# Optimization experiments

Hardware: AMD Instinct MI355X
Metric: run time of the kernel (lower is better)

Reference implementation:

```python
import jax, jax.numpy as jnp
import numpy as np
from jax import lax

SLOPE = 0.01  # nn.LeakyReLU default negative slope

def leaky(x):
    return jnp.where(x >= 0, x, SLOPE * x)

def conv2d(x, w, b, pad):
    # x: [N,C,H,W], w: [O,I,kh,kw]
    y = lax.conv_general_dilated(x, w, (1, 1), [(pad, pad), (pad, pad)],
                                 dimension_numbers=('NCHW', 'OIHW', 'NCHW'))
    return y + b[None, :, None, None]

def centered_ifftn(x, axes):
    # np.fft.fftshift(np.fft.ifftn(np.fft.ifftshift(X), norm='ortho'))
    return jnp.fft.fftshift(jnp.fft.ifftn(jnp.fft.ifftshift(x, axes=axes), axes=axes, norm='ortho'), axes=axes)

def setup_inputs() -> dict:
    key = jax.random.key(0)
    ks = jax.random.split(key, 10)
    B, H, W, CK = 8, 640, 368, 32
    return {
        'img':    jax.random.normal(ks[0], (B, 1, H, W), jnp.float32),
        'kspace': jax.random.normal(ks[1], (B, 2, H, W), jnp.float32),
        # k_model1: Conv2d(2, CK, 3, padding=1) + LeakyReLU
        'wk': jax.random.normal(ks[2], (CK, 2, 3, 3), jnp.float32) * 0.1,
        'bk': jnp.zeros((CK,), jnp.float32),
        # conv1: Conv2d(CK, 2, kernel_size=1)
        'w1': jax.random.normal(ks[3], (2, CK, 1, 1), jnp.float32) * 0.1,
        'b1': jnp.zeros((2,), jnp.float32),
        # conv2: Conv2d(2, 1, kernel_size=1)
        'w2': jax.random.normal(ks[4], (1, 2, 1, 1), jnp.float32) * 0.1,
        'b2': jnp.zeros((1,), jnp.float32),
        # i_model1: Conv2d(1, 1, 3, padding=1) + LeakyReLU
        'wi': jax.random.normal(ks[5], (1, 1, 3, 3), jnp.float32) * 0.1,
        'bi': jnp.zeros((1,), jnp.float32),
    }

def reference(img, kspace, wk, bk, w1, b1, w2, b2, wi, bi):
    # k-space branch: k_model1 then conv1 + LeakyReLU
    out1 = leaky(conv2d(leaky(conv2d(kspace, wk, bk, 1)), w1, b1, 0))  # [B,2,H,W]
    # channel 0 = real, channel 1 = imag; ifftn over ALL axes (incl. batch),
    # exactly as the original numpy call with axes=range(out.ndim)
    cplx = out1[:, 0].astype(jnp.complex64) + 1j * out1[:, 1].astype(jnp.complex64)  # [B,H,W]
    im = jnp.abs(centered_ifftn(cplx, (0, 1, 2)))[:, None]  # [B,1,H,W]
    # concat with image, cast to half (torch.cuda.HalfTensor), conv2 + LeakyReLU
    out = jnp.concatenate([im, img], axis=1).astype(jnp.float16)  # [B,2,H,W]
    out = leaky(conv2d(out, w2.astype(jnp.float16), b2.astype(jnp.float16), 0))
    out = out.astype(jnp.float32)  # [B,1,H,W]
    # image-domain model
    return leaky(conv2d(out, wi, bi, 1))  # [B,1,H,W]
```

## Files before the change

kernel.cpp:

```cpp
#include <hip/hip_runtime.h>
#include <hip/hip_fp16.h>
#include <math.h>

#define B_ 8
#define H_ 640
#define W_ 368
#define HW_ (H_*W_)
#define NP_ (B_*H_*W_)

#define FROWS 4
#define HP 645
#define TS 16

typedef __attribute__((ext_vector_type(8))) short v8s;
typedef __attribute__((ext_vector_type(4))) float v4f;

__device__ __forceinline__ float leaky_(float x){ return fmaxf(x, 0.01f*x); }

__device__ __forceinline__ unsigned short f2bf(float x){
    unsigned u = __float_as_uint(x);
    u += 0x7FFFu + ((u >> 16) & 1u);
    return (unsigned short)(u >> 16);
}

__device__ __forceinline__ float2 cadd_(float2 a, float2 b){ return make_float2(a.x+b.x, a.y+b.y); }
__device__ __forceinline__ float2 csub_(float2 a, float2 b){ return make_float2(a.x-b.x, a.y-b.y); }
__device__ __forceinline__ float2 cmul_(float2 a, float c, float s){
    return make_float2(a.x*c - a.y*s, a.x*s + a.y*c);
}
__device__ __forceinline__ float2 cmulv_(float2 a, float2 w){
    return make_float2(a.x*w.x - a.y*w.y, a.x*w.y + a.y*w.x);
}

__device__ __forceinline__ void dft4p_(float2 p0, float2 p1, float2 p2, float2 p3,
                                       float2& z0, float2& z1, float2& z2, float2& z3){
    float2 s0 = cadd_(p0,p2), d0 = csub_(p0,p2);
    float2 s1 = cadd_(p1,p3), d1 = csub_(p1,p3);
    z0 = cadd_(s0,s1);
    z2 = csub_(s0,s1);
    z1 = make_float2(d0.x - d1.y, d0.y + d1.x);
    z3 = make_float2(d0.x + d1.y, d0.y - d1.x);
}

__device__ __forceinline__ void fft16p_(const float2* x, float2* X){
    const float C1 = 0.9238795325112867f, S1 = 0.3826834323650898f;
    const float R  = 0.7071067811865476f;
    float2 Y[4][4];
    #pragma unroll
    for (int b = 0; b < 4; ++b)
        dft4p_(x[b], x[4+b], x[8+b], x[12+b], Y[b][0], Y[b][1], Y[b][2], Y[b][3]);
    Y[1][1] = cmul_(Y[1][1],  C1,  S1);
    Y[1][2] = cmul_(Y[1][2],   R,   R);
    Y[1][3] = cmul_(Y[1][3],  S1,  C1);
    Y[2][1] = cmul_(Y[2][1],   R,   R);
    Y[2][2] = make_float2(-Y[2][2].y, Y[2][2].x);
    Y[2][3] = cmul_(Y[2][3],  -R,   R);
    Y[3][1] = cmul_(Y[3][1],  S1,  C1);
    Y[3][2] = cmul_(Y[3][2],  -R,   R);
    Y[3][3] = cmul_(Y[3][3], -C1, -S1);
    #pragma unroll
    for (int c = 0; c < 4; ++c)
        dft4p_(Y[0][c], Y[1][c], Y[2][c], Y[3][c], X[c], X[c+4], X[c+8], X[c+12]);
}

__device__ __forceinline__ void fft8p_(const float2* x, float2* X){
    const float R = 0.7071067811865476f;
    float2 Y0[4], Y1[4];
    dft4p_(x[0], x[2], x[4], x[6], Y0[0], Y0[1], Y0[2], Y0[3]);
    dft4p_(x[1], x[3], x[5], x[7], Y1[0], Y1[1], Y1[2], Y1[3]);
    float2 T0 = Y1[0];
    float2 T1 = cmul_(Y1[1],  R, R);
    float2 T2 = make_float2(-Y1[2].y, Y1[2].x);
    float2 T3 = cmul_(Y1[3], -R, R);
    X[0] = cadd_(Y0[0], T0);  X[4] = csub_(Y0[0], T0);
    X[1] = cadd_(Y0[1], T1);  X[5] = csub_(Y0[1], T1);
    X[2] = cadd_(Y0[2], T2);  X[6] = csub_(Y0[2], T2);
    X[3] = cadd_(Y0[3], T3);  X[7] = csub_(Y0[3], T3);
}

__global__ void init_tables_kernel(float2* __restrict__ T){
    int i = blockIdx.x*blockDim.x + threadIdx.x;
    if (i >= 1301) return;
    int r, c, modN; int j;
    if      (i <  368){ j = i;        r = j%16; c = j/16; modN = 368; }
    else if (i < 1008){ j = i-368;    r = j%16; c = j/16; modN = 640; }
    else if (i < 1048){ j = i-1008;   r = j%8;  c = j/8;  modN = 40;  }
    else              { j = i-1048;   r = j/11; c = j%11 + 1; modN = 23; }
    int t = (int)(((long long)r * c) % modN);
    if (t > modN/2) t -= modN;
    float ang = (float)(6.283185307179586 * ((double)t / (double)modN));
    float s, co;
    sincosf(ang, &s, &co);
    T[i] = make_float2(co, s);
}

__global__ __launch_bounds__(512) void kfftw_kernel(const float* __restrict__ ksp,
                               const float* __restrict__ wk,
                               const float* __restrict__ bk,
                               const float* __restrict__ w1,
                               const float* __restrict__ b1,
                               const float2* __restrict__ TW368P,
                               const float2* __restrict__ F23P,
                               float2* __restrict__ Bt){
    __shared__ unsigned short Sb[4836];
    __shared__ unsigned short Wr[8*512];
    __shared__ float2 X[FROWS*369];
    int t = threadIdx.x;
    int blk = blockIdx.x;
    int b  = blk / 160;
    int h0 = (blk - b*160) * FROWS;

    for (int seg = 0; seg < 12; ++seg){
        int r = seg >> 1, ic = seg & 1;
        int hh = h0 - 1 + r;
        int ok = ((unsigned)hh < 640u);
        const float* base = ksp + ((size_t)(b*2 + ic)*640 + (ok ? hh : 0))*368;
        for (int col = t; col < 372; col += 512){
            int c = col - 1;
            float v = (ok && (unsigned)c < 368u) ? base[c] : 0.f;
            Sb[seg*372 + col] = f2bf(v);
        }
    }
    for (int i = t; i < 372; i += 512) Sb[4464 + i] = 0;

    int lane = t & 63, wave = t >> 6;
    int oc = lane & 15, q = lane >> 4;
    int l = wave >> 1, half = wave & 1;

    int off[8];
    v8s bf0, bf1, b2f;
    #pragma unroll
    for (int j = 0; j < 8; ++j){
        int kk = q*8 + j;
        if (kk < 18){
            int ic = (kk >= 9) ? 1 : 0;
            int tt = kk - ic*9;
            int ty = tt/3, tx = tt - ty*3;
            off[j] = ((ty + l)*2 + ic)*372 + tx;
            bf0[j] = (short)f2bf(wk[oc*18 + kk]);
            bf1[j] = (short)f2bf(wk[(oc+16)*18 + kk]);
        } else {
            off[j] = 4464;
            bf0[j] = 0; bf1[j] = 0;
        }
        b2f[j] = (oc < 2) ? (short)f2bf(w1[oc*32 + kk]) : (short)0;
    }
    float bk0 = bk[oc], bk1 = bk[oc+16];
    float biasn = (oc == 1) ? b1[1] : b1[0];
    unsigned short* Wrw = Wr + (wave << 9);
    __syncthreads();

    int gbeg = half ? 12 : 0;
    int gend = half ? 23 : 12;
    for (int g = gbeg; g < gend; ++g){
        int w0m = g*16 + oc;
        v8s af;
        #pragma unroll
        for (int j = 0; j < 8; ++j) af[j] = (short)Sb[off[j] + w0m];
        v4f d0 = {0.f,0.f,0.f,0.f}, d1 = {0.f,0.f,0.f,0.f};
        d0 = __builtin_amdgcn_mfma_f32_16x16x32_bf16(af, bf0, d0, 0, 0, 0);
        d1 = __builtin_amdgcn_mfma_f32_16x16x32_bf16(af, bf1, d1, 0, 0, 0);
        #pragma unroll
        for (int r = 0; r < 4; ++r){
            int px = q*4 + r;
            Wrw[px*32 + oc]      = f2bf(leaky_(d0[r] + bk0));
            Wrw[px*32 + 16 + oc] = f2bf(leaky_(d1[r] + bk1));
        }
        asm volatile("s_waitcnt lgkmcnt(0)" ::: "memory");
        const v8s* ap = (const v8s*)(Wrw + oc*32);
        v8s a2 = ap[q];
        v4f d2 = {0.f,0.f,0.f,0.f};
        d2 = __builtin_amdgcn_mfma_f32_16x16x32_bf16(a2, b2f, d2, 0, 0, 0);
        float vals[4], ov[4];
        #pragma unroll
        for (int r = 0; r < 4; ++r){
            vals[r] = leaky_(biasn + d2[r]);
            ov[r] = __shfl_xor(vals[r], 1);
        }
        if (oc == 0){
            int px = g*16 + q*4;
            X[l*369 + px  ] = make_float2( vals[0],  ov[0]);
            X[l*369 + px+1] = make_float2(-vals[1], -ov[1]);
            X[l*369 + px+2] = make_float2( vals[2],  ov[2]);
            X[l*369 + px+3] = make_float2(-vals[3], -ov[3]);
        }
        asm volatile("s_waitcnt lgkmcnt(0)" ::: "memory");
    }
    __syncthreads();

    if (t < 92){
        int ll = t & 3, n2 = t >> 2;
        float2 xr[16], Xo[16];
        #pragma unroll
        for (int n1 = 0; n1 < 16; ++n1) xr[n1] = X[ll*369 + 23*n1 + n2];
        fft16p_(xr, Xo);
        const float2* row = TW368P + n2*16;
        #pragma unroll
        for (int k1 = 0; k1 < 16; ++k1)
            X[ll*369 + 23*k1 + n2] = cmulv_(Xo[k1], row[k1]);
    }
    __syncthreads();

    {
        int k1 = t & 15, ll = (t >> 4) & 3, eighth = t >> 6;
        const float2* xp = X + ll*369 + 23*k1;
        float2 x0 = xp[0];
        float2 u[11], d[11];
        #pragma unroll
        for (int m = 1; m <= 11; ++m){
            float2 a = xp[m], bb = xp[23-m];
            u[m-1] = cadd_(a, bb);
            d[m-1] = csub_(a, bb);
        }
        __syncthreads();
        int k2beg = eighth*3;
        int k2end = min(k2beg + 3, 23);
        for (int k2 = k2beg; k2 < k2end; ++k2){
            const float2* row = F23P + k2*11;
            float re = x0.x, im = x0.y;
            #pragma unroll
            for (int m = 0; m < 11; ++m){
                float c = row[m].x, s = row[m].y;
                re += u[m].x*c - d[m].y*s;
                im += u[m].y*c + d[m].x*s;
            }
            X[ll*369 + k1 + 16*k2] = make_float2(re, im);
        }
    }
    __syncthreads();

    const float sc = 0.052129458158616354f;
    for (int i = t; i < FROWS*368; i += 512){
        int k = i >> 2, ll = i & 3;
        float2 v = X[ll*369 + k];
        float s = (k & 1) ? -sc : sc;
        Bt[((size_t)(b*368 + k))*640 + h0 + ll] = make_float2(v.x*s, v.y*s);
    }
}

__global__ __launch_bounds__(256) void ffthb_kernel(const float2* __restrict__ Bt,
                                                    const float2* __restrict__ TW640P,
                                                    const float2* __restrict__ TW40P,
                                                    float* __restrict__ Mag){
    __shared__ float2 X[8*HP];
    int t = threadIdx.x;
    int w = blockIdx.x;

    for (int i = t; i < 8*640; i += 256){
        int l = i / 640, n = i - l*640;
        float2 v = Bt[((size_t)(l*368 + w))*640 + n];
        float s = (n & 1) ? -1.f : 1.f;
        X[l*HP + n] = make_float2(v.x*s, v.y*s);
    }
    __syncthreads();

    for (int it = t; it < 320; it += 256){
        int l = it & 7, n2 = it >> 3;
        float2 xr[16], Xo[16];
        #pragma unroll
        for (int n1 = 0; n1 < 16; ++n1) xr[n1] = X[l*HP + 40*n1 + n2];
        fft16p_(xr, Xo);
        const float2* row = TW640P + n2*16;
        #pragma unroll
        for (int k1 = 0; k1 < 16; ++k1)
            X[l*HP + 40*k1 + n2] = cmulv_(Xo[k1], row[k1]);
    }
    __syncthreads();

    for (int it = t; it < 640; it += 256){
        int l = it & 7, k1 = (it >> 3) & 15, m2 = it >> 7;
        float2 xr[8], Xo[8];
        #pragma unroll
        for (int m1 = 0; m1 < 8; ++m1) xr[m1] = X[l*HP + 40*k1 + 5*m1 + m2];
        fft8p_(xr, Xo);
        const float2* row = TW40P + m2*8;
        #pragma unroll
        for (int j1 = 0; j1 < 8; ++j1)
            X[l*HP + 40*k1 + 5*j1 + m2] = cmulv_(Xo[j1], row[j1]);
    }
    __syncthreads();

    {
        const float CK1[5] = {1.f,  0.30901699437494745f, -0.8090169943749475f, -0.8090169943749475f,  0.30901699437494745f};
        const float SK1[5] = {0.f,  0.9510565162951535f,   0.5877852522924731f, -0.5877852522924731f, -0.9510565162951535f};
        const float CK2[5] = {1.f, -0.8090169943749475f,   0.30901699437494745f, 0.30901699437494745f, -0.8090169943749475f};
        const float SK2[5] = {0.f,  0.5877852522924731f,  -0.9510565162951535f,  0.9510565162951535f, -0.5877852522924731f};
        float2 p[4][5];
        int ui[4];
        #pragma unroll
        for (int i = 0; i < 4; ++i){
            int u = t + 256*i;
            ui[u >= 1024 ? 0 : i] = u;
            ui[i] = u;
            int l = u & 7, k1 = (u >> 3) & 15, j1 = u >> 7;
            #pragma unroll
            for (int m2 = 0; m2 < 5; ++m2)
                p[i][m2] = X[l*HP + 40*k1 + 5*j1 + m2];
        }
        __syncthreads();
        #pragma unroll
        for (int i = 0; i < 4; ++i){
            int u = ui[i];
            int l = u & 7, k1 = (u >> 3) & 15, j1 = u >> 7;
            float2 ua = cadd_(p[i][1], p[i][4]), da = csub_(p[i][1], p[i][4]);
            float2 ub = cadd_(p[i][2], p[i][3]), db = csub_(p[i][2], p[i][3]);
            #pragma unroll
            for (int j2 = 0; j2 < 5; ++j2){
                float c1v = CK1[j2], s1v = SK1[j2], c2v = CK2[j2], s2v = SK2[j2];
                float re = p[i][0].x + ua.x*c1v - da.y*s1v + ub.x*c2v - db.y*s2v;
                float im = p[i][0].y + ua.y*c1v + da.x*s1v + ub.y*c2v + db.x*s2v;
                X[l*HP + k1 + 16*j1 + 128*j2] = make_float2(re, im);
            }
        }
    }
    __syncthreads();

    const float SC = 0.013975424859373685f;
    for (int hh = t; hh < 640; hh += 256){
        float2 x[8], Xo[8];
        #pragma unroll
        for (int l = 0; l < 8; ++l){
            float2 v = X[l*HP + hh];
            float s = (l & 1) ? -SC : SC;
            x[l] = make_float2(v.x*s, v.y*s);
        }
        fft8p_(x, Xo);
        #pragma unroll
        for (int k = 0; k < 8; ++k){
            float mag = sqrtf(Xo[k].x*Xo[k].x + Xo[k].y*Xo[k].y);
            Mag[((size_t)(k*368 + w))*640 + hh] = mag;
        }
    }
}

__global__ __launch_bounds__(256) void tail_kernel(const float* __restrict__ Mag,
                                  const float* __restrict__ img,
                                  const float* __restrict__ w2,
                                  const float* __restrict__ b2,
                                  const float* __restrict__ wi,
                                  const float* __restrict__ bi,
                                  float* __restrict__ out){
    __shared__ float Pl[8][TS+2][TS+3];
    int t = threadIdx.x;
    int ty0 = (blockIdx.x / 23) * TS;
    int tx0 = (blockIdx.x % 23) * TS;

    float w2h0 = __half2float(__float2half(w2[0]));
    float w2h1 = __half2float(__float2half(w2[1]));
    float b2h  = __half2float(__float2half(b2[0]));

    for (int idx = t; idx < (TS+2)*(TS+2); idx += 256){
        int hx = idx / (TS+2), hy = idx - hx*(TS+2);
        int hh = ty0 - 1 + hy, ww = tx0 - 1 + hx;
        int hc = min(max(hh, 0), H_-1), wc = min(max(ww, 0), W_-1);
        #pragma unroll
        for (int k = 0; k < 8; ++k){
            float mag = Mag[((size_t)(k*368 + wc))*640 + hc];
            Pl[k][hy][hx] = __half2float(__float2half(mag));
        }
    }
    __syncthreads();

    for (int idx = t; idx < (TS+2)*(TS+2); idx += 256){
        int hy = idx / (TS+2), hx = idx - hy*(TS+2);
        int hh = ty0 - 1 + hy, ww = tx0 - 1 + hx;
        bool inb = (hh >= 0) && (hh < H_) && (ww >= 0) && (ww < W_);
        int hc = min(max(hh, 0), H_-1), wc = min(max(ww, 0), W_-1);
        float inbf = inb ? 1.f : 0.f;
        #pragma unroll
        for (int k = 0; k < 8; ++k){
            float g = __half2float(__float2half(img[(size_t)k*HW_ + hc*W_ + wc]));
            float a = Pl[k][hy][hx];
            float o = leaky_(a*w2h0 + g*w2h1 + b2h);
            o = __half2float(__float2half(o));
            Pl[k][hy][hx] = o * inbf;
        }
    }
    __syncthreads();

    int sy = t >> 4, sx = t & 15;
    float wv[9];
    #pragma unroll
    for (int q = 0; q < 9; ++q) wv[q] = wi[q];
    float bi0 = bi[0];
    #pragma unroll
    for (int k = 0; k < 8; ++k){
        float acc = bi0;
        #pragma unroll
        for (int dy = 0; dy < 3; ++dy)
            #pragma unroll
            for (int dx = 0; dx < 3; ++dx)
                acc += wv[dy*3+dx] * Pl[k][sy+dy][sx+dx];
        out[((size_t)k*H_ + ty0+sy)*W_ + tx0+sx] = leaky_(acc);
    }
}

extern "C" void kernel_launch(void* const* d_in, const int* in_sizes, int n_in,
                              void* d_out, int out_size, void* d_ws, size_t ws_size,
                              hipStream_t stream){
    const float* img = (const float*)d_in[0];
    const float* ksp = (const float*)d_in[1];
    const float* wk  = (const float*)d_in[2];
    const float* bk  = (const float*)d_in[3];
    const float* w1  = (const float*)d_in[4];
    const float* b1  = (const float*)d_in[5];
    const float* w2  = (const float*)d_in[6];
    const float* b2  = (const float*)d_in[7];
    const float* wi  = (const float*)d_in[8];
    const float* bi  = (const float*)d_in[9];

    char* ws = (char*)d_ws;
    float2* Bt  = (float2*)(ws + 0);
    float*  Mag = (float*)(ws + 15073280);
    float2* T   = (float2*)(ws + 30146560);
    float2* TW368P = T + 0;
    float2* TW640P = T + 368;
    float2* TW40P  = T + 1008;
    float2* F23P   = T + 1048;
    float* out  = (float*)d_out;

    init_tables_kernel<<<6, 256, 0, stream>>>(T);

    kfftw_kernel<<<B_*(H_/FROWS), 512, 0, stream>>>(ksp, wk, bk, w1, b1,
                                                    TW368P, F23P, Bt);
    ffthb_kernel<<<W_, 256, 0, stream>>>(Bt, TW640P, TW40P, Mag);
    tail_kernel<<<(H_/TS)*(W_/TS), 256, 0, stream>>>(Mag, img, w2, b2, wi, bi, out);
}
```

Baseline: 191.0 us.

## Rebalance thread counts and make per-wave FFT stages sync-free in height kernel

```diff
diff --git a/kernel.cpp b/kernel.cpp
--- a/kernel.cpp
+++ b/kernel.cpp
@@ -94,7 +94,7 @@
     T[i] = make_float2(co, s);
 }
 
-__global__ __launch_bounds__(512) void kfftw_kernel(const float* __restrict__ ksp,
+__global__ __launch_bounds__(256) void kfftw_kernel(const float* __restrict__ ksp,
                                const float* __restrict__ wk,
                                const float* __restrict__ bk,
                                const float* __restrict__ w1,
@@ -103,7 +103,7 @@
                                const float2* __restrict__ F23P,
                                float2* __restrict__ Bt){
     __shared__ unsigned short Sb[4836];
-    __shared__ unsigned short Wr[8*512];
+    __shared__ unsigned short Wr[4*512];
     __shared__ float2 X[FROWS*369];
     int t = threadIdx.x;
     int blk = blockIdx.x;
@@ -115,17 +115,17 @@
         int hh = h0 - 1 + r;
         int ok = ((unsigned)hh < 640u);
         const float* base = ksp + ((size_t)(b*2 + ic)*640 + (ok ? hh : 0))*368;
-        for (int col = t; col < 372; col += 512){
+        for (int col = t; col < 372; col += 256){
             int c = col - 1;
             float v = (ok && (unsigned)c < 368u) ? base[c] : 0.f;
             Sb[seg*372 + col] = f2bf(v);
         }
     }
-    for (int i = t; i < 372; i += 512) Sb[4464 + i] = 0;
+    for (int i = t; i < 372; i += 256) Sb[4464 + i] = 0;
 
     int lane = t & 63, wave = t >> 6;
     int oc = lane & 15, q = lane >> 4;
-    int l = wave >> 1, half = wave & 1;
+    int l = wave;
 
     int off[8];
     v8s bf0, bf1, b2f;
@@ -150,9 +150,7 @@
     unsigned short* Wrw = Wr + (wave << 9);
     __syncthreads();
 
-    int gbeg = half ? 12 : 0;
-    int gend = half ? 23 : 12;
-    for (int g = gbeg; g < gend; ++g){
+    for (int g = 0; g < 23; ++g){
         int w0m = g*16 + oc;
         v8s af;
         #pragma unroll
@@ -202,7 +200,7 @@
     __syncthreads();
 
     {
-        int k1 = t & 15, ll = (t >> 4) & 3, eighth = t >> 6;
+        int ll = t & 3, k1 = (t >> 2) & 15, qr = t >> 6;
         const float2* xp = X + ll*369 + 23*k1;
         float2 x0 = xp[0];
         float2 u[11], d[11];
@@ -213,8 +211,8 @@
             d[m-1] = csub_(a, bb);
         }
         __syncthreads();
-        int k2beg = eighth*3;
-        int k2end = min(k2beg + 3, 23);
+        int k2beg = qr*6;
+        int k2end = (qr == 3) ? 23 : k2beg + 6;
         for (int k2 = k2beg; k2 < k2end; ++k2){
             const float2* row = F23P + k2*11;
             float re = x0.x, im = x0.y;
@@ -230,7 +228,7 @@
     __syncthreads();
 
     const float sc = 0.052129458158616354f;
-    for (int i = t; i < FROWS*368; i += 512){
+    for (int i = t; i < FROWS*368; i += 256){
         int k = i >> 2, ll = i & 3;
         float2 v = X[ll*369 + k];
         float s = (k & 1) ? -sc : sc;
@@ -238,91 +236,89 @@
     }
 }
 
-__global__ __launch_bounds__(256) void ffthb_kernel(const float2* __restrict__ Bt,
+__global__ __launch_bounds__(512) void ffthb_kernel(const float2* __restrict__ Bt,
                                                     const float2* __restrict__ TW640P,
                                                     const float2* __restrict__ TW40P,
                                                     float* __restrict__ Mag){
     __shared__ float2 X[8*HP];
     int t = threadIdx.x;
+    int lane = t & 63, l = t >> 6;
     int w = blockIdx.x;
-
-    for (int i = t; i < 8*640; i += 256){
-        int l = i / 640, n = i - l*640;
-        float2 v = Bt[((size_t)(l*368 + w))*640 + n];
+    float2* Xl = X + l*HP;
+
+    const float2* src = Bt + ((size_t)(l*368 + w))*640;
+    for (int n = lane; n < 640; n += 64){
+        float2 v = src[n];
         float s = (n & 1) ? -1.f : 1.f;
-        X[l*HP + n] = make_float2(v.x*s, v.y*s);
-    }
-    __syncthreads();
-
-    for (int it = t; it < 320; it += 256){
-        int l = it & 7, n2 = it >> 3;
+        Xl[n] = make_float2(v.x*s, v.y*s);
+    }
+    asm volatile("s_waitcnt vmcnt(0) lgkmcnt(0)" ::: "memory");
+
+    if (lane < 40){
+        int n2 = lane;
         float2 xr[16], Xo[16];
         #pragma unroll
-        for (int n1 = 0; n1 < 16; ++n1) xr[n1] = X[l*HP + 40*n1 + n2];
+        for (int n1 = 0; n1 < 16; ++n1) xr[n1] = Xl[40*n1 + n2];
         fft16p_(xr, Xo);
         const float2* row = TW640P + n2*16;
         #pragma unroll
         for (int k1 = 0; k1 < 16; ++k1)
-            X[l*HP + 40*k1 + n2] = cmulv_(Xo[k1], row[k1]);
-    }
-    __syncthreads();
-
-    for (int it = t; it < 640; it += 256){
-        int l = it & 7, k1 = (it >> 3) & 15, m2 = it >> 7;
+            Xl[40*k1 + n2] = cmulv_(Xo[k1], row[k1]);
+    }
+    asm volatile("s_waitcnt lgkmcnt(0)" ::: "memory");
+
+    for (int it = lane; it < 80; it += 64){
+        int k1 = it & 15, m2 = it >> 4;
         float2 xr[8], Xo[8];
         #pragma unroll
-        for (int m1 = 0; m1 < 8; ++m1) xr[m1] = X[l*HP + 40*k1 + 5*m1 + m2];
+        for (int m1 = 0; m1 < 8; ++m1) xr[m1] = Xl[40*k1 + 5*m1 + m2];
         fft8p_(xr, Xo);
         const float2* row = TW40P + m2*8;
         #pragma unroll
         for (int j1 = 0; j1 < 8; ++j1)
-            X[l*HP + 40*k1 + 5*j1 + m2] = cmulv_(Xo[j1], row[j1]);
-    }
-    __syncthreads();
+            Xl[40*k1 + 5*j1 + m2] = cmulv_(Xo[j1], row[j1]);
+    }
+    asm volatile("s_waitcnt lgkmcnt(0)" ::: "memory");
 
     {
         const float CK1[5] = {1.f,  0.30901699437494745f, -0.8090169943749475f, -0.8090169943749475f,  0.30901699437494745f};
         const float SK1[5] = {0.f,  0.9510565162951535f,   0.5877852522924731f, -0.5877852522924731f, -0.9510565162951535f};
         const float CK2[5] = {1.f, -0.8090169943749475f,   0.30901699437494745f, 0.30901699437494745f, -0.8090169943749475f};
         const float SK2[5] = {0.f,  0.5877852522924731f,  -0.9510565162951535f,  0.9510565162951535f, -0.5877852522924731f};
-        float2 p[4][5];
-        int ui[4];
-        #pragma unroll
-        for (int i = 0; i < 4; ++i){
-            int u = t + 256*i;
-            ui[u >= 1024 ? 0 : i] = u;
-            ui[i] = u;
-            int l = u & 7, k1 = (u >> 3) & 15, j1 = u >> 7;
-            #pragma unroll
-            for (int m2 = 0; m2 < 5; ++m2)
-                p[i][m2] = X[l*HP + 40*k1 + 5*j1 + m2];
-        }
-        __syncthreads();
-        #pragma unroll
-        for (int i = 0; i < 4; ++i){
-            int u = ui[i];
-            int l = u & 7, k1 = (u >> 3) & 15, j1 = u >> 7;
-            float2 ua = cadd_(p[i][1], p[i][4]), da = csub_(p[i][1], p[i][4]);
-            float2 ub = cadd_(p[i][2], p[i][3]), db = csub_(p[i][2], p[i][3]);
-            #pragma unroll
-            for (int j2 = 0; j2 < 5; ++j2){
-                float c1v = CK1[j2], s1v = SK1[j2], c2v = CK2[j2], s2v = SK2[j2];
-                float re = p[i][0].x + ua.x*c1v - da.y*s1v + ub.x*c2v - db.y*s2v;
-                float im = p[i][0].y + ua.y*c1v + da.x*s1v + ub.y*c2v + db.x*s2v;
-                X[l*HP + k1 + 16*j1 + 128*j2] = make_float2(re, im);
-            }
+        int itA = lane, itB = lane + 64;
+        int kA = itA & 15, jA = itA >> 4;
+        int kB = itB & 15, jB = itB >> 4;
+        float2 pA[5], pB[5];
+        #pragma unroll
+        for (int m2 = 0; m2 < 5; ++m2) pA[m2] = Xl[40*kA + 5*jA + m2];
+        #pragma unroll
+        for (int m2 = 0; m2 < 5; ++m2) pB[m2] = Xl[40*kB + 5*jB + m2];
+        asm volatile("s_waitcnt lgkmcnt(0)" ::: "memory");
+        float2 uAa = cadd_(pA[1], pA[4]), dAa = csub_(pA[1], pA[4]);
+        float2 uAb = cadd_(pA[2], pA[3]), dAb = csub_(pA[2], pA[3]);
+        float2 uBa = cadd_(pB[1], pB[4]), dBa = csub_(pB[1], pB[4]);
+        float2 uBb = cadd_(pB[2], pB[3]), dBb = csub_(pB[2], pB[3]);
+        #pragma unroll
+        for (int j2 = 0; j2 < 5; ++j2){
+            float c1v = CK1[j2], s1v = SK1[j2], c2v = CK2[j2], s2v = SK2[j2];
+            float reA = pA[0].x + uAa.x*c1v - dAa.y*s1v + uAb.x*c2v - dAb.y*s2v;
+            float imA = pA[0].y + uAa.y*c1v + dAa.x*s1v + uAb.y*c2v + dAb.x*s2v;
+            float reB = pB[0].x + uBa.x*c1v - dBa.y*s1v + uBb.x*c2v - dBb.y*s2v;
+            float imB = pB[0].y + uBa.y*c1v + dBa.x*s1v + uBb.y*c2v + dBb.x*s2v;
+            Xl[kA + 16*jA + 128*j2] = make_float2(reA, imA);
+            Xl[kB + 16*jB + 128*j2] = make_float2(reB, imB);
         }
     }
     __syncthreads();
 
     const float SC = 0.013975424859373685f;
-    for (int hh = t; hh < 640; hh += 256){
+    for (int hh = t; hh < 640; hh += 512){
         float2 x[8], Xo[8];
         #pragma unroll
-        for (int l = 0; l < 8; ++l){
-            float2 v = X[l*HP + hh];
-            float s = (l & 1) ? -SC : SC;
-            x[l] = make_float2(v.x*s, v.y*s);
+        for (int ll = 0; ll < 8; ++ll){
+            float2 v = X[ll*HP + hh];
+            float s = (ll & 1) ? -SC : SC;
+            x[ll] = make_float2(v.x*s, v.y*s);
         }
         fft8p_(x, Xo);
         #pragma unroll
@@ -421,8 +417,8 @@
 
     init_tables_kernel<<<6, 256, 0, stream>>>(T);
 
-    kfftw_kernel<<<B_*(H_/FROWS), 512, 0, stream>>>(ksp, wk, bk, w1, b1,
+    kfftw_kernel<<<B_*(H_/FROWS), 256, 0, stream>>>(ksp, wk, bk, w1, b1,
                                                     TW368P, F23P, Bt);
-    ffthb_kernel<<<W_, 256, 0, stream>>>(Bt, TW640P, TW40P, Mag);
+    ffthb_kernel<<<W_, 512, 0, stream>>>(Bt, TW640P, TW40P, Mag);
     tail_kernel<<<(H_/TS)*(W_/TS), 256, 0, stream>>>(Mag, img, w2, b2, wi, bi, out);
 }
```

New measurement: 172.6 us. 1.11x faster.
